# Kernel tuning notes

Measured on AMD Instinct MI355X. Metric: run time of the kernel, lower is better.

The kernel has to match this reference:

```python
import jax, jax.numpy as jnp
import numpy as np

D_KEY = 512
D_VALUE = 512
D_MEM_HIDDEN = 64
BATCH = 65536


def setup_inputs() -> dict:
    key = jax.random.key(0)
    ks = jax.random.split(key, 6)
    return {
        "key": jax.random.normal(ks[0], (BATCH, D_KEY), dtype=jnp.float32),
        "value": jax.random.normal(ks[1], (BATCH, D_VALUE), dtype=jnp.float32),
        # memory MLP weights (the stored memory)
        "mem_W1": jax.random.normal(ks[2], (D_MEM_HIDDEN, D_KEY), dtype=jnp.float32) * 0.02,
        "mem_b1": jnp.zeros((D_MEM_HIDDEN,), dtype=jnp.float32),
        "mem_W2": jax.random.normal(ks[3], (D_VALUE, D_MEM_HIDDEN), dtype=jnp.float32) * 0.02,
        "mem_b2": jnp.zeros((D_VALUE,), dtype=jnp.float32),
        # per-dimension precision head
        "prec_W": jax.random.normal(ks[4], (D_VALUE, D_KEY), dtype=jnp.float32) * 0.01,
        "prec_b": jnp.ones((D_VALUE,), dtype=jnp.float32),
    }


def reference(key, value, mem_W1, mem_b1, mem_W2, mem_b2, prec_W, prec_b):
    """Faithful translation of MemoryModule.free_energy.

    F = prec * clamp(value - pred, -3, 3)^2 - log(prec), averaged over d_value.
    """
    # predict: two-layer MLP with exact (erf) GELU, matching torch F.gelu default
    h = jax.nn.gelu(key @ mem_W1.T + mem_b1, approximate=False)  # (B, H)
    pred = h @ mem_W2.T + mem_b2                                  # (B, Dv)
    # precision head: softplus + 0.01, always positive
    prec = jax.nn.softplus(key @ prec_W.T + prec_b) + 0.01        # (B, Dv)
    error = jnp.clip(value - pred, -3.0, 3.0)                     # (B, Dv)
    F_per_dim = prec * error * error - jnp.log(prec)
    F_scalar = F_per_dim.mean(axis=-1)                            # (B,)
    return (F_scalar, pred, prec, error)
```

## Files before the change

### kernel.cpp

```cpp
#include <hip/hip_runtime.h>
#include <hip/hip_bf16.h>

#define BATCH 65536
#define DK 512
#define DV 512
#define DH 64
#define BMR 16
#define NIT 8

typedef __attribute__((ext_vector_type(8))) short bf16x8;
typedef __attribute__((ext_vector_type(4))) float f32x4;

__device__ __align__(16) short g_wb[327680];

__device__ __forceinline__ short f2bf(float f) {
    union { __hip_bfloat16 h; short s; } u;
    u.h = __float2bfloat16(f);
    return u.s;
}

__device__ __forceinline__ bf16x8 pack8(float4 a, float4 b) {
    bf16x8 r;
    r[0] = f2bf(a.x); r[1] = f2bf(a.y); r[2] = f2bf(a.z); r[3] = f2bf(a.w);
    r[4] = f2bf(b.x); r[5] = f2bf(b.y); r[6] = f2bf(b.z); r[7] = f2bf(b.w);
    return r;
}

__global__ __launch_bounds__(256) void conv_weights(
    const float* __restrict__ W1, const float* __restrict__ W2,
    const float* __restrict__ Wp)
{
    int f = blockIdx.x * 256 + threadIdx.x;
    int lane = f & 63;
    const float* src; int stride, row, col;
    if (f < 4096) {
        int t = f >> 10, kk = (f >> 6) & 15;
        src = W1; stride = DK;
        row = t * 16 + (lane & 15); col = kk * 32 + (lane >> 4) * 8;
    } else if (f < 8192) {
        int g = f - 4096; int t = g >> 7, kh = (g >> 6) & 1;
        src = W2; stride = DH;
        row = t * 16 + (lane & 15); col = kh * 32 + (lane >> 4) * 8;
    } else {
        int g = f - 8192; int t = g >> 10, kk = (g >> 6) & 15;
        src = Wp; stride = DK;
        row = t * 16 + (lane & 15); col = kk * 32 + (lane >> 4) * 8;
    }
    const float* p = src + (long)row * stride + col;
    float4 a = *reinterpret_cast<const float4*>(p);
    float4 b = *reinterpret_cast<const float4*>(p + 4);
    *reinterpret_cast<bf16x8*>(g_wb + (long)f * 8) = pack8(a, b);
}

__global__ __launch_bounds__(256, 3) void fused_free_energy(
    const float* __restrict__ key, const float* __restrict__ value,
    const float* __restrict__ b1, const float* __restrict__ b2,
    const float* __restrict__ pb,
    float* __restrict__ outF, float* __restrict__ outPred,
    float* __restrict__ outPrec, float* __restrict__ outErr)
{
    __shared__ __align__(16) char xbuf[32768];

    const bf16x8* W1F = reinterpret_cast<const bf16x8*>(g_wb);
    const bf16x8* W2F = reinterpret_cast<const bf16x8*>(g_wb + 32768);
    const bf16x8* WpF = reinterpret_cast<const bf16x8*>(g_wb + 65536);

    const int tid  = threadIdx.x;
    const int wave = tid >> 6;
    const int lane = tid & 63;
    const int lh   = lane & 15;
    const int lg   = lane >> 4;
    const long row0 = (long)blockIdx.x * BMR;
    const f32x4 zf = {0.f, 0.f, 0.f, 0.f};

    bf16x8 kreg[16];
    {
        const float* krow = key + (row0 + lh) * DK + lg * 8;
        #pragma unroll
        for (int kk = 0; kk < 16; ++kk) {
            float4 a = *reinterpret_cast<const float4*>(krow + kk * 32);
            float4 b = *reinterpret_cast<const float4*>(krow + kk * 32 + 4);
            kreg[kk] = pack8(a, b);
        }
    }

    short hs_all[16];
    #pragma unroll
    for (int jt = 0; jt < 4; ++jt) {
        f32x4 aE = zf, aO = zf;
        #pragma unroll
        for (int kk = 0; kk < 16; kk += 2) {
            bf16x8 f0 = W1F[(jt * 16 + kk) * 64 + lane];
            bf16x8 f1 = W1F[(jt * 16 + kk + 1) * 64 + lane];
            aE = __builtin_amdgcn_mfma_f32_16x16x32_bf16(f0, kreg[kk],     aE, 0, 0, 0);
            aO = __builtin_amdgcn_mfma_f32_16x16x32_bf16(f1, kreg[kk + 1], aO, 0, 0, 0);
        }
        float4 b1v = *reinterpret_cast<const float4*>(b1 + jt * 16 + lg * 4);
        float b1a[4] = {b1v.x, b1v.y, b1v.z, b1v.w};
        #pragma unroll
        for (int r = 0; r < 4; ++r) {
            float z = aE[r] + aO[r] + b1a[r];
            float g = 0.5f * z * (1.0f + erff(z * 0.70710678f));
            hs_all[jt * 4 + r] = f2bf(g);
        }
    }
    #pragma unroll
    for (int jt = 0; jt < 4; ++jt) {
        int hb = wave * 2048 + ((lh * 128 + jt * 32 + lg * 8) ^ ((lh & 7) << 4));
        short4 hv = {hs_all[jt * 4 + 0], hs_all[jt * 4 + 1],
                     hs_all[jt * 4 + 2], hs_all[jt * 4 + 3]};
        *reinterpret_cast<short4*>(xbuf + hb) = hv;
    }
    __syncthreads();
    bf16x8 hreg[2];
    #pragma unroll
    for (int kh = 0; kh < 2; ++kh) {
        int byte = (lh * 128 + kh * 64 + lg * 16) ^ ((lh & 7) << 4);
        hreg[kh] = *reinterpret_cast<const bf16x8*>(xbuf + wave * 2048 + byte);
    }
    __syncthreads();

    f32x4 predz[NIT], z3v[NIT];
    #pragma unroll
    for (int it = 0; it < NIT; ++it) {
        const int tile = wave * NIT + it;
        f32x4 aE = zf, aO = zf;
        #pragma unroll
        for (int kk = 0; kk < 16; kk += 2) {
            bf16x8 f0 = WpF[(tile * 16 + kk) * 64 + lane];
            bf16x8 f1 = WpF[(tile * 16 + kk + 1) * 64 + lane];
            aE = __builtin_amdgcn_mfma_f32_16x16x32_bf16(f0, kreg[kk],     aE, 0, 0, 0);
            aO = __builtin_amdgcn_mfma_f32_16x16x32_bf16(f1, kreg[kk + 1], aO, 0, 0, 0);
        }
        f32x4 acc2 = zf;
        #pragma unroll
        for (int kh = 0; kh < 2; ++kh) {
            bf16x8 f = W2F[(tile * 2 + kh) * 64 + lane];
            acc2 = __builtin_amdgcn_mfma_f32_16x16x32_bf16(f, hreg[kh], acc2, 0, 0, 0);
        }
        int nb = tile * 16 + lg * 4;
        float4 b2v = *reinterpret_cast<const float4*>(b2 + nb);
        float4 pbv = *reinterpret_cast<const float4*>(pb + nb);
        f32x4 pz, zz;
        pz[0] = acc2[0] + b2v.x; pz[1] = acc2[1] + b2v.y;
        pz[2] = acc2[2] + b2v.z; pz[3] = acc2[3] + b2v.w;
        zz[0] = aE[0] + aO[0] + pbv.x; zz[1] = aE[1] + aO[1] + pbv.y;
        zz[2] = aE[2] + aO[2] + pbv.z; zz[3] = aE[3] + aO[3] + pbv.w;
        predz[it] = pz; z3v[it] = zz;
    }

    #pragma unroll
    for (int it = 0; it < NIT; ++it) {
        int cb = (wave * 512 + it * 64 + lg * 16) ^ ((lh & 15) << 4);
        *reinterpret_cast<f32x4*>(xbuf + lh * 2048 + cb) = predz[it];
    }
    __syncthreads();
    float4 errs[NIT];
    float  fp[NIT];
    #pragma unroll
    for (int p = 0; p < NIT; ++p) {
        int row = wave * 4 + (p >> 1);
        int ob  = (p & 1) * 1024 + lane * 16;
        int rb  = ob ^ ((row & 15) << 4);
        float4 pr = *reinterpret_cast<const float4*>(xbuf + row * 2048 + rb);
        long ga = (row0 + row) * (long)DV + (ob >> 2);
        float4 va = *reinterpret_cast<const float4*>(value + ga);
        float4 er;
        er.x = fminf(fmaxf(va.x - pr.x, -3.f), 3.f);
        er.y = fminf(fmaxf(va.y - pr.y, -3.f), 3.f);
        er.z = fminf(fmaxf(va.z - pr.z, -3.f), 3.f);
        er.w = fminf(fmaxf(va.w - pr.w, -3.f), 3.f);
        errs[p] = er;
        *reinterpret_cast<float4*>(outPred + ga) = pr;
    }
    __syncthreads();

    #pragma unroll
    for (int it = 0; it < NIT; ++it) {
        int cb = (wave * 512 + it * 64 + lg * 16) ^ ((lh & 15) << 4);
        *reinterpret_cast<f32x4*>(xbuf + lh * 2048 + cb) = z3v[it];
    }
    __syncthreads();
    #pragma unroll
    for (int p = 0; p < NIT; ++p) {
        int row = wave * 4 + (p >> 1);
        int ob  = (p & 1) * 1024 + lane * 16;
        int rb  = ob ^ ((row & 15) << 4);
        float4 zz = *reinterpret_cast<const float4*>(xbuf + row * 2048 + rb);
        long ga = (row0 + row) * (long)DV + (ob >> 2);
        float za[4] = {zz.x, zz.y, zz.z, zz.w};
        float ea[4] = {errs[p].x, errs[p].y, errs[p].z, errs[p].w};
        float pc[4], f = 0.f;
        #pragma unroll
        for (int r = 0; r < 4; ++r) {
            float z = za[r];
            float prec = fmaxf(z, 0.f) + __logf(1.0f + __expf(-fabsf(z))) + 0.01f;
            pc[r] = prec;
            f += prec * ea[r] * ea[r] - __logf(prec);
        }
        fp[p] = f;
        float4 pc4 = {pc[0], pc[1], pc[2], pc[3]};
        *reinterpret_cast<float4*>(outPrec + ga) = pc4;
        *reinterpret_cast<float4*>(outErr  + ga) = errs[p];
    }

    #pragma unroll
    for (int rr = 0; rr < 4; ++rr) {
        float s = fp[2 * rr] + fp[2 * rr + 1];
        #pragma unroll
        for (int off = 1; off < 64; off <<= 1)
            s += __shfl_xor(s, off, 64);
        if (lane == 0) outF[row0 + wave * 4 + rr] = s * (1.0f / 512.0f);
    }
}

extern "C" void kernel_launch(void* const* d_in, const int* in_sizes, int n_in,
                              void* d_out, int out_size, void* d_ws, size_t ws_size,
                              hipStream_t stream) {
    const float* key   = (const float*)d_in[0];
    const float* value = (const float*)d_in[1];
    const float* W1    = (const float*)d_in[2];
    const float* b1    = (const float*)d_in[3];
    const float* W2    = (const float*)d_in[4];
    const float* b2    = (const float*)d_in[5];
    const float* Wp    = (const float*)d_in[6];
    const float* pb    = (const float*)d_in[7];

    float* outF    = (float*)d_out;
    float* outPred = outF + BATCH;
    float* outPrec = outPred + (long)BATCH * DV;
    float* outErr  = outPrec + (long)BATCH * DV;

    conv_weights<<<160, 256, 0, stream>>>(W1, W2, Wp);
    fused_free_energy<<<BATCH / BMR, 256, 0, stream>>>(key, value, b1, b2, pb,
                                                       outF, outPred, outPrec, outErr);
}
```

Before: 300.0 us.

## Stage key in LDS and stream output tiles in chunks to raise occupancy

Key rows are no longer held in sixteen bf16x8 registers per lane. They are converted once into a swizzled LDS buffer, and MFMA B-fragments are read from there. The precision/prediction phase now runs as four sequential column chunks that go through LDS, with a fused epilogue per chunk, instead of holding eight pred and z accumulators per wave. This cuts register pressure, so launch bounds rise from 3 to 4 blocks per SIMD; in exchange the kernel does repeated LDS fragment reads and more block-wide barriers.

```diff
diff --git a/kernel.cpp b/kernel.cpp
--- a/kernel.cpp
+++ b/kernel.cpp
@@ -6,7 +6,6 @@
 #define DV 512
 #define DH 64
 #define BMR 16
-#define NIT 8
 
 typedef __attribute__((ext_vector_type(8))) short bf16x8;
 typedef __attribute__((ext_vector_type(4))) float f32x4;
@@ -52,14 +51,18 @@
     *reinterpret_cast<bf16x8*>(g_wb + (long)f * 8) = pack8(a, b);
 }
 
-__global__ __launch_bounds__(256, 3) void fused_free_energy(
+#define KOF 0
+#define XP  16384
+#define XZ  24576
+
+__global__ __launch_bounds__(256, 4) void fused_free_energy(
     const float* __restrict__ key, const float* __restrict__ value,
     const float* __restrict__ b1, const float* __restrict__ b2,
     const float* __restrict__ pb,
     float* __restrict__ outF, float* __restrict__ outPred,
     float* __restrict__ outPrec, float* __restrict__ outErr)
 {
-    __shared__ __align__(16) char xbuf[32768];
+    __shared__ __align__(16) char lds[32768];
 
     const bf16x8* W1F = reinterpret_cast<const bf16x8*>(g_wb);
     const bf16x8* W2F = reinterpret_cast<const bf16x8*>(g_wb + 32768);
@@ -73,144 +76,135 @@
     const long row0 = (long)blockIdx.x * BMR;
     const f32x4 zf = {0.f, 0.f, 0.f, 0.f};
 
-    bf16x8 kreg[16];
     {
-        const float* krow = key + (row0 + lh) * DK + lg * 8;
-        #pragma unroll
-        for (int kk = 0; kk < 16; ++kk) {
-            float4 a = *reinterpret_cast<const float4*>(krow + kk * 32);
-            float4 b = *reinterpret_cast<const float4*>(krow + kk * 32 + 4);
-            kreg[kk] = pack8(a, b);
-        }
-    }
-
-    short hs_all[16];
+        #pragma unroll
+        for (int i = 0; i < 4; ++i) {
+            int idx = i * 256 + tid;
+            int r = idx >> 6, c8 = idx & 63;
+            const float* p = key + (row0 + r) * DK + c8 * 8;
+            float4 a = *reinterpret_cast<const float4*>(p);
+            float4 b = *reinterpret_cast<const float4*>(p + 4);
+            int byte = (r * 1024 + c8 * 16) ^ ((r & 7) << 4);
+            *reinterpret_cast<bf16x8*>(lds + KOF + byte) = pack8(a, b);
+        }
+    }
+    __syncthreads();
+
+    #define KFRAG(kk) (*reinterpret_cast<const bf16x8*>( \
+        lds + KOF + ((lh * 1024 + (kk) * 64 + lg * 16) ^ ((lh & 7) << 4))))
+
+    bf16x8 hreg[2];
+    {
+        short hs_all[16];
+        #pragma unroll
+        for (int jt = 0; jt < 4; ++jt) {
+            f32x4 aE = zf, aO = zf;
+            #pragma unroll
+            for (int kk = 0; kk < 16; kk += 2) {
+                bf16x8 f0 = W1F[(jt * 16 + kk) * 64 + lane];
+                bf16x8 f1 = W1F[(jt * 16 + kk + 1) * 64 + lane];
+                aE = __builtin_amdgcn_mfma_f32_16x16x32_bf16(f0, KFRAG(kk),     aE, 0, 0, 0);
+                aO = __builtin_amdgcn_mfma_f32_16x16x32_bf16(f1, KFRAG(kk + 1), aO, 0, 0, 0);
+            }
+            float4 b1v = *reinterpret_cast<const float4*>(b1 + jt * 16 + lg * 4);
+            float b1a[4] = {b1v.x, b1v.y, b1v.z, b1v.w};
+            #pragma unroll
+            for (int r = 0; r < 4; ++r) {
+                float z = aE[r] + aO[r] + b1a[r];
+                float g = 0.5f * z * (1.0f + erff(z * 0.70710678f));
+                hs_all[jt * 4 + r] = f2bf(g);
+            }
+        }
+        #pragma unroll
+        for (int jt = 0; jt < 4; ++jt) {
+            int hb = XP + wave * 2048 + ((lh * 128 + jt * 32 + lg * 8) ^ ((lh & 7) << 4));
+            short4 hv = {hs_all[jt * 4 + 0], hs_all[jt * 4 + 1],
+                         hs_all[jt * 4 + 2], hs_all[jt * 4 + 3]};
+            *reinterpret_cast<short4*>(lds + hb) = hv;
+        }
+        __syncthreads();
+        #pragma unroll
+        for (int kh = 0; kh < 2; ++kh) {
+            int byte = (lh * 128 + kh * 64 + lg * 16) ^ ((lh & 7) << 4);
+            hreg[kh] = *reinterpret_cast<const bf16x8*>(lds + XP + wave * 2048 + byte);
+        }
+        __syncthreads();
+    }
+
+    float facc0 = 0.f, facc1 = 0.f;
+    #pragma unroll 1
+    for (int ot = 0; ot < 4; ++ot) {
+        #pragma unroll
+        for (int sub = 0; sub < 2; ++sub) {
+            const int tt = ot * 8 + wave * 2 + sub;
+            f32x4 aE = zf, aO = zf;
+            #pragma unroll
+            for (int kk = 0; kk < 16; kk += 2) {
+                bf16x8 f0 = WpF[(tt * 16 + kk) * 64 + lane];
+                bf16x8 f1 = WpF[(tt * 16 + kk + 1) * 64 + lane];
+                aE = __builtin_amdgcn_mfma_f32_16x16x32_bf16(f0, KFRAG(kk),     aE, 0, 0, 0);
+                aO = __builtin_amdgcn_mfma_f32_16x16x32_bf16(f1, KFRAG(kk + 1), aO, 0, 0, 0);
+            }
+            f32x4 acc2 = zf;
+            #pragma unroll
+            for (int kh = 0; kh < 2; ++kh) {
+                bf16x8 f = W2F[(tt * 2 + kh) * 64 + lane];
+                acc2 = __builtin_amdgcn_mfma_f32_16x16x32_bf16(f, hreg[kh], acc2, 0, 0, 0);
+            }
+            int nb = tt * 16 + lg * 4;
+            float4 b2v = *reinterpret_cast<const float4*>(b2 + nb);
+            float4 pbv = *reinterpret_cast<const float4*>(pb + nb);
+            f32x4 pz, zz;
+            pz[0] = acc2[0] + b2v.x; pz[1] = acc2[1] + b2v.y;
+            pz[2] = acc2[2] + b2v.z; pz[3] = acc2[3] + b2v.w;
+            zz[0] = aE[0] + aO[0] + pbv.x; zz[1] = aE[1] + aO[1] + pbv.y;
+            zz[2] = aE[2] + aO[2] + pbv.z; zz[3] = aE[3] + aO[3] + pbv.w;
+            int relb = (wave * 2 + sub) * 64 + lg * 16;
+            int sb = (lh * 512 + relb) ^ ((lh & 7) << 4);
+            *reinterpret_cast<f32x4*>(lds + XP + sb) = pz;
+            *reinterpret_cast<f32x4*>(lds + XZ + sb) = zz;
+        }
+        __syncthreads();
+
+        #pragma unroll
+        for (int ch = 0; ch < 2; ++ch) {
+            int row  = wave * 4 + (lane >> 5) + ch * 2;
+            int colb = (lane & 31) * 16;
+            int rb   = (row * 512 + colb) ^ ((row & 7) << 4);
+            float4 pr = *reinterpret_cast<const float4*>(lds + XP + rb);
+            float4 zz = *reinterpret_cast<const float4*>(lds + XZ + rb);
+            long ga = (row0 + row) * (long)DV + ot * 128 + (lane & 31) * 4;
+            float4 va = *reinterpret_cast<const float4*>(value + ga);
+            float pa[4] = {pr.x, pr.y, pr.z, pr.w};
+            float za[4] = {zz.x, zz.y, zz.z, zz.w};
+            float vaa[4] = {va.x, va.y, va.z, va.w};
+            float er[4], pc[4], f = 0.f;
+            #pragma unroll
+            for (int r = 0; r < 4; ++r) {
+                float z = za[r];
+                float prec = fmaxf(z, 0.f) + __logf(1.0f + __expf(-fabsf(z))) + 0.01f;
+                float e = fminf(fmaxf(vaa[r] - pa[r], -3.f), 3.f);
+                pc[r] = prec; er[r] = e;
+                f += prec * e * e - __logf(prec);
+            }
+            float4 pc4 = {pc[0], pc[1], pc[2], pc[3]};
+            float4 er4 = {er[0], er[1], er[2], er[3]};
+            *reinterpret_cast<float4*>(outPred + ga) = pr;
+            *reinterpret_cast<float4*>(outPrec + ga) = pc4;
+            *reinterpret_cast<float4*>(outErr  + ga) = er4;
+            if (ch == 0) facc0 += f; else facc1 += f;
+        }
+        __syncthreads();
+    }
+
     #pragma unroll
-    for (int jt = 0; jt < 4; ++jt) {
-        f32x4 aE = zf, aO = zf;
-        #pragma unroll
-        for (int kk = 0; kk < 16; kk += 2) {
-            bf16x8 f0 = W1F[(jt * 16 + kk) * 64 + lane];
-            bf16x8 f1 = W1F[(jt * 16 + kk + 1) * 64 + lane];
-            aE = __builtin_amdgcn_mfma_f32_16x16x32_bf16(f0, kreg[kk],     aE, 0, 0, 0);
-            aO = __builtin_amdgcn_mfma_f32_16x16x32_bf16(f1, kreg[kk + 1], aO, 0, 0, 0);
-        }
-        float4 b1v = *reinterpret_cast<const float4*>(b1 + jt * 16 + lg * 4);
-        float b1a[4] = {b1v.x, b1v.y, b1v.z, b1v.w};
-        #pragma unroll
-        for (int r = 0; r < 4; ++r) {
-            float z = aE[r] + aO[r] + b1a[r];
-            float g = 0.5f * z * (1.0f + erff(z * 0.70710678f));
-            hs_all[jt * 4 + r] = f2bf(g);
-        }
-    }
-    #pragma unroll
-    for (int jt = 0; jt < 4; ++jt) {
-        int hb = wave * 2048 + ((lh * 128 + jt * 32 + lg * 8) ^ ((lh & 7) << 4));
-        short4 hv = {hs_all[jt * 4 + 0], hs_all[jt * 4 + 1],
-                     hs_all[jt * 4 + 2], hs_all[jt * 4 + 3]};
-        *reinterpret_cast<short4*>(xbuf + hb) = hv;
-    }
-    __syncthreads();
-    bf16x8 hreg[2];
-    #pragma unroll
-    for (int kh = 0; kh < 2; ++kh) {
-        int byte = (lh * 128 + kh * 64 + lg * 16) ^ ((lh & 7) << 4);
-        hreg[kh] = *reinterpret_cast<const bf16x8*>(xbuf + wave * 2048 + byte);
-    }
-    __syncthreads();
-
-    f32x4 predz[NIT], z3v[NIT];
-    #pragma unroll
-    for (int it = 0; it < NIT; ++it) {
-        const int tile = wave * NIT + it;
-        f32x4 aE = zf, aO = zf;
-        #pragma unroll
-        for (int kk = 0; kk < 16; kk += 2) {
-            bf16x8 f0 = WpF[(tile * 16 + kk) * 64 + lane];
-            bf16x8 f1 = WpF[(tile * 16 + kk + 1) * 64 + lane];
-            aE = __builtin_amdgcn_mfma_f32_16x16x32_bf16(f0, kreg[kk],     aE, 0, 0, 0);
-            aO = __builtin_amdgcn_mfma_f32_16x16x32_bf16(f1, kreg[kk + 1], aO, 0, 0, 0);
-        }
-        f32x4 acc2 = zf;
-        #pragma unroll
-        for (int kh = 0; kh < 2; ++kh) {
-            bf16x8 f = W2F[(tile * 2 + kh) * 64 + lane];
-            acc2 = __builtin_amdgcn_mfma_f32_16x16x32_bf16(f, hreg[kh], acc2, 0, 0, 0);
-        }
-        int nb = tile * 16 + lg * 4;
-        float4 b2v = *reinterpret_cast<const float4*>(b2 + nb);
-        float4 pbv = *reinterpret_cast<const float4*>(pb + nb);
-        f32x4 pz, zz;
-        pz[0] = acc2[0] + b2v.x; pz[1] = acc2[1] + b2v.y;
-        pz[2] = acc2[2] + b2v.z; pz[3] = acc2[3] + b2v.w;
-        zz[0] = aE[0] + aO[0] + pbv.x; zz[1] = aE[1] + aO[1] + pbv.y;
-        zz[2] = aE[2] + aO[2] + pbv.z; zz[3] = aE[3] + aO[3] + pbv.w;
-        predz[it] = pz; z3v[it] = zz;
-    }
-
-    #pragma unroll
-    for (int it = 0; it < NIT; ++it) {
-        int cb = (wave * 512 + it * 64 + lg * 16) ^ ((lh & 15) << 4);
-        *reinterpret_cast<f32x4*>(xbuf + lh * 2048 + cb) = predz[it];
-    }
-    __syncthreads();
-    float4 errs[NIT];
-    float  fp[NIT];
-    #pragma unroll
-    for (int p = 0; p < NIT; ++p) {
-        int row = wave * 4 + (p >> 1);
-        int ob  = (p & 1) * 1024 + lane * 16;
-        int rb  = ob ^ ((row & 15) << 4);
-        float4 pr = *reinterpret_cast<const float4*>(xbuf + row * 2048 + rb);
-        long ga = (row0 + row) * (long)DV + (ob >> 2);
-        float4 va = *reinterpret_cast<const float4*>(value + ga);
-        float4 er;
-        er.x = fminf(fmaxf(va.x - pr.x, -3.f), 3.f);
-        er.y = fminf(fmaxf(va.y - pr.y, -3.f), 3.f);
-        er.z = fminf(fmaxf(va.z - pr.z, -3.f), 3.f);
-        er.w = fminf(fmaxf(va.w - pr.w, -3.f), 3.f);
-        errs[p] = er;
-        *reinterpret_cast<float4*>(outPred + ga) = pr;
-    }
-    __syncthreads();
-
-    #pragma unroll
-    for (int it = 0; it < NIT; ++it) {
-        int cb = (wave * 512 + it * 64 + lg * 16) ^ ((lh & 15) << 4);
-        *reinterpret_cast<f32x4*>(xbuf + lh * 2048 + cb) = z3v[it];
-    }
-    __syncthreads();
-    #pragma unroll
-    for (int p = 0; p < NIT; ++p) {
-        int row = wave * 4 + (p >> 1);
-        int ob  = (p & 1) * 1024 + lane * 16;
-        int rb  = ob ^ ((row & 15) << 4);
-        float4 zz = *reinterpret_cast<const float4*>(xbuf + row * 2048 + rb);
-        long ga = (row0 + row) * (long)DV + (ob >> 2);
-        float za[4] = {zz.x, zz.y, zz.z, zz.w};
-        float ea[4] = {errs[p].x, errs[p].y, errs[p].z, errs[p].w};
-        float pc[4], f = 0.f;
-        #pragma unroll
-        for (int r = 0; r < 4; ++r) {
-            float z = za[r];
-            float prec = fmaxf(z, 0.f) + __logf(1.0f + __expf(-fabsf(z))) + 0.01f;
-            pc[r] = prec;
-            f += prec * ea[r] * ea[r] - __logf(prec);
-        }
-        fp[p] = f;
-        float4 pc4 = {pc[0], pc[1], pc[2], pc[3]};
-        *reinterpret_cast<float4*>(outPrec + ga) = pc4;
-        *reinterpret_cast<float4*>(outErr  + ga) = errs[p];
-    }
-
-    #pragma unroll
-    for (int rr = 0; rr < 4; ++rr) {
-        float s = fp[2 * rr] + fp[2 * rr + 1];
-        #pragma unroll
-        for (int off = 1; off < 64; off <<= 1)
+    for (int ch = 0; ch < 2; ++ch) {
+        float s = (ch == 0) ? facc0 : facc1;
+        #pragma unroll
+        for (int off = 1; off < 32; off <<= 1)
             s += __shfl_xor(s, off, 64);
-        if (lane == 0) outF[row0 + wave * 4 + rr] = s * (1.0f / 512.0f);
+        if ((lane & 31) == 0)
+            outF[row0 + wave * 4 + (lane >> 5) + ch * 2] = s * (1.0f / 512.0f);
     }
 }
 
```

Measured after the change: 272.1 us. 9.3% less time.
